# Optimization experiments

Measured on AMD Instinct MI355X. Metric: run time of the kernel, lower is better.

Reference implementation:

```python
import jax, jax.numpy as jnp
import numpy as np


def gcn_layer(h, src, dst, norm, W, b, num_nodes):
    # PyG GCNConv: linear transform, normalized scatter-add aggregation, then bias
    h = h @ W                                    # [N, out]
    msg = h[src] * norm[:, None]                 # [E+N, out] gathered messages
    out = jax.ops.segment_sum(msg, dst, num_segments=num_nodes)
    return out + b


def setup_inputs() -> dict:
    key = jax.random.key(0)
    ks = jax.random.split(key, 6)
    N, E, D, H, C = 100000, 1600000, 128, 64, 2
    x = jax.random.normal(ks[0], (N, D), dtype=jnp.float32)
    edge_index = jax.random.randint(ks[1], (2, E), 0, N, dtype=jnp.int64)
    def glorot(k, shape):
        lim = np.sqrt(6.0 / (shape[0] + shape[1]))
        return jax.random.uniform(k, shape, jnp.float32, -lim, lim)
    return {
        "x": x,
        "edge_index": edge_index,
        "W1": glorot(ks[2], (D, H)), "b1": jnp.zeros((H,), jnp.float32),
        "W2": glorot(ks[3], (H, H)), "b2": jnp.zeros((H,), jnp.float32),
        "W3": glorot(ks[4], (H, H)), "b3": jnp.zeros((H,), jnp.float32),
        "Wfc": glorot(ks[5], (H, C)), "bfc": jnp.zeros((C,), jnp.float32),
    }


def reference(x, edge_index, W1, b1, W2, b2, W3, b3, Wfc, bfc):
    N = x.shape[0]
    # add self loops (GCNConv default), symmetric deg^-1/2 normalization
    loops = jnp.arange(N, dtype=edge_index.dtype)
    src = jnp.concatenate([edge_index[0], loops])
    dst = jnp.concatenate([edge_index[1], loops])
    deg = jax.ops.segment_sum(jnp.ones_like(dst, dtype=x.dtype), dst, num_segments=N)
    dinv = jnp.where(deg > 0, jax.lax.rsqrt(deg), 0.0)
    norm = dinv[src] * dinv[dst]

    h = jax.nn.relu(gcn_layer(x, src, dst, norm, W1, b1, N))
    h = jax.nn.relu(gcn_layer(h, src, dst, norm, W2, b2, N))
    h = jax.nn.relu(gcn_layer(h, src, dst, norm, W3, b3, N))
    logits = h @ Wfc + bfc
    return jax.nn.log_softmax(logits, axis=1)
```

## Files before the change

### kernel.cpp

```cpp
#include <hip/hip_runtime.h>
#include <math.h>


static inline size_t alignup(size_t x){ return (x + 511) & ~size_t(511); }

typedef float v4f __attribute__((ext_vector_type(4)));
typedef unsigned short v4u16 __attribute__((ext_vector_type(4)));

__device__ __forceinline__ unsigned short f32_to_bf16(float f){
  union { float f; unsigned int u; } c; c.f = f;
  unsigned int u = c.u + 0x7FFFu + ((c.u >> 16) & 1u);
  return (unsigned short)(u >> 16);
}
__device__ __forceinline__ v4f bf16x4_to_f32(v4u16 a){
  union { unsigned int u; float f; } c0,c1,c2,c3;
  c0.u = (unsigned int)a.x << 16;
  c1.u = (unsigned int)a.y << 16;
  c2.u = (unsigned int)a.z << 16;
  c3.u = (unsigned int)a.w << 16;
  v4f r; r.x=c0.f; r.y=c1.f; r.z=c2.f; r.w=c3.f;
  return r;
}

#define NBUCK 1024
#define CHUNK 8192
#define CCAP  3584

__global__ void zero_kernel(int* __restrict__ p, int n){
  int i = blockIdx.x*256 + threadIdx.x;
  if(i<n) p[i] = 0;
}

__global__ __launch_bounds__(1024) void hist_kernel(const int* __restrict__ dst,
                                                    int* __restrict__ bcnt, int E){
  __shared__ int h[NBUCK];
  int t = threadIdx.x;
  h[t]=0;
  __syncthreads();
  int base = blockIdx.x*CHUNK;
  #pragma unroll
  for(int i=0;i<CHUNK;i+=1024){
    int e = base+i+t;
    if(e<E) atomicAdd(&h[dst[e]>>7], 1);
  }
  __syncthreads();
  if(h[t]) atomicAdd(&bcnt[t], h[t]);
}

__global__ void scan_buckets_kernel(const int* __restrict__ bcnt, int* __restrict__ bbase,
                                    int* __restrict__ bfill){
  __shared__ int sh[256];
  int t = threadIdx.x;
  int v0=bcnt[4*t], v1=bcnt[4*t+1], v2=bcnt[4*t+2], v3=bcnt[4*t+3];
  int ts = v0+v1+v2+v3;
  sh[t]=ts; __syncthreads();
  for(int off=1; off<256; off<<=1){
    int x=(t>=off)?sh[t-off]:0; __syncthreads();
    sh[t]+=x; __syncthreads();
  }
  int run = sh[t]-ts;
  int i0=4*t;
  bbase[i0+0]=run; bfill[i0+0]=run; run+=v0;
  bbase[i0+1]=run; bfill[i0+1]=run; run+=v1;
  bbase[i0+2]=run; bfill[i0+2]=run; run+=v2;
  bbase[i0+3]=run; bfill[i0+3]=run;
}

__global__ __launch_bounds__(1024) void scatter_kernel(const int* __restrict__ src,
                                                       const int* __restrict__ dst,
                                                       int* __restrict__ bfill,
                                                       int* __restrict__ pairs, int E){
  __shared__ int hist[NBUCK];
  __shared__ int delta[NBUCK];
  __shared__ int wsum[16];
  __shared__ int vals[CHUNK];
  __shared__ unsigned short bkt[CHUNK];
  int t = threadIdx.x;
  int lane = t & 63, wid = t >> 6;
  int cbase = blockIdx.x*CHUNK;
  hist[t]=0;
  __syncthreads();
  #pragma unroll
  for(int i=0;i<CHUNK;i+=1024){
    int e = cbase+i+t;
    if(e<E) atomicAdd(&hist[dst[e]>>7], 1);
  }
  __syncthreads();
  int v = hist[t];
  int x = v;
  #pragma unroll
  for(int off=1; off<64; off<<=1){
    int y = __shfl_up(x, off, 64);
    if(lane >= off) x += y;
  }
  if(lane==63) wsum[wid]=x;
  __syncthreads();
  if(wid==0){
    int s2 = (lane<16) ? wsum[lane] : 0;
    #pragma unroll
    for(int off=1; off<16; off<<=1){
      int y = __shfl_up(s2, off, 64);
      if(lane >= off) s2 += y;
    }
    if(lane<16) wsum[lane]=s2;
  }
  __syncthreads();
  int run = (x - v) + (wid ? wsum[wid-1] : 0);
  int g = v ? atomicAdd(&bfill[t], v) : 0;
  hist[t]=run; delta[t]=g-run;
  __syncthreads();
  #pragma unroll
  for(int i=0;i<CHUNK;i+=1024){
    int e = cbase+i+t;
    if(e<E){
      int d = dst[e];
      int b = d>>7;
      int slot = atomicAdd(&hist[b], 1);
      vals[slot] = ((d&127)<<17) | src[e];
      bkt[slot]  = (unsigned short)b;
    }
  }
  __syncthreads();
  int cnt = E - cbase; if(cnt > CHUNK) cnt = CHUNK;
  for(int i=t;i<cnt;i+=1024){
    int b = bkt[i];
    pairs[delta[b] + i] = vals[i];
  }
}

__global__ __launch_bounds__(256) void bucket_csr_kernel(const int* __restrict__ pairs,
                                                         const int* __restrict__ bbase,
                                                         int* __restrict__ row_ptr,
                                                         float* __restrict__ dinv,
                                                         int* __restrict__ col,
                                                         int N, int E){
  __shared__ int hist[128];
  __shared__ int pref[128];
  __shared__ int fill[128];
  __shared__ int srcs[CCAP];
  int b = blockIdx.x, t = threadIdx.x;
  int s = bbase[b], e = bbase[b+1];
  int cnt = e - s; if(cnt > CCAP) cnt = CCAP;
  if(t<128) hist[t]=0;
  __syncthreads();
  int v[CCAP/256];
  #pragma unroll
  for(int i=0;i<CCAP/256;i++){
    int idx = i*256 + t;
    if(idx<cnt){ v[i]=pairs[s+idx]; atomicAdd(&hist[v[i]>>17], 1); }
  }
  __syncthreads();
  if(t<128) pref[t]=hist[t];
  __syncthreads();
  for(int off=1; off<128; off<<=1){
    int x=0;
    if(t<128 && t>=off) x=pref[t-off];
    __syncthreads();
    if(t<128) pref[t]+=x;
    __syncthreads();
  }
  if(t<128){
    int ex = pref[t]-hist[t];
    fill[t]=ex;
    int node = b*128 + t;
    if(node<N){
      row_ptr[node] = s + ex;
      dinv[node] = rsqrtf((float)(hist[t]+1));
    }
  }
  if(b==0 && t==0) row_ptr[N]=E;
  __syncthreads();
  #pragma unroll
  for(int i=0;i<CCAP/256;i++){
    int idx = i*256 + t;
    if(idx<cnt){
      int ld = v[i]>>17;
      int pos = atomicAdd(&fill[ld], 1);
      srcs[pos] = v[i] & 0x1FFFF;
    }
  }
  __syncthreads();
  for(int i=t;i<cnt;i+=256) col[s+i]=srcs[i];
}

template<int K>
__global__ __launch_bounds__(256) void lin_kernel(const float* __restrict__ h,
                                                  const float* __restrict__ W,
                                                  const float* __restrict__ dinv,
                                                  unsigned short* __restrict__ g, int N){
  constexpr int TR = 32, RW = 8;
  __shared__ __align__(16) float hs[TR*K];
  __shared__ __align__(16) float ws[K*64];
  int t = threadIdx.x, wave = t>>6, lane = t&63;
  long rbase = (long)blockIdx.x*TR;
  const v4f* wsrc = (const v4f*)W;
  #pragma unroll
  for(int idx = t; idx < K*16; idx += 256)
    ((v4f*)ws)[idx] = wsrc[idx];
  const v4f* hsrc = (const v4f*)(h + rbase*K);
  if(rbase + TR <= N){
    #pragma unroll
    for(int idx = t; idx < TR*K/4; idx += 256)
      ((v4f*)hs)[idx] = hsrc[idx];
  } else {
    int lim = (int)((N - rbase)*K/4);
    for(int idx = t; idx < lim; idx += 256)
      ((v4f*)hs)[idx] = hsrc[idx];
  }
  __syncthreads();
  float acc[RW];
  #pragma unroll
  for(int r=0;r<RW;r++) acc[r]=0.f;
  const float* hw = hs + wave*RW*K;
  #pragma unroll 2
  for(int k=0;k<K;k+=4){
    float w0 = ws[(k+0)*64+lane];
    float w1 = ws[(k+1)*64+lane];
    float w2 = ws[(k+2)*64+lane];
    float w3 = ws[(k+3)*64+lane];
    #pragma unroll
    for(int r=0;r<RW;r++){
      v4f hv = *(const v4f*)&hw[r*K+k];
      acc[r] = fmaf(hv.w, w3, fmaf(hv.z, w2, fmaf(hv.y, w1, fmaf(hv.x, w0, acc[r]))));
    }
  }
  long row0 = rbase + wave*RW;
  #pragma unroll
  for(int r=0;r<RW;r++){
    if(row0 + r < N)
      g[(row0+r)*64 + lane] = f32_to_bf16(dinv[row0+r]*acc[r]);
  }
}

__device__ __forceinline__ v4f gather_row4(const unsigned short* __restrict__ g,
                                           const int* __restrict__ col,
                                           int n, int s, int e, int l){
  v4f acc = bf16x4_to_f32(*(const v4u16*)&g[(size_t)n*64 + l*4]);
  for(int i = s; i < e; i += 16){
    int rem = e - i;
    int myc = (l < rem) ? col[i + l] : n;
    #pragma unroll
    for(int j0 = 0; j0 < 16; j0 += 4){
      int c0 = __shfl(myc, j0+0, 16);
      int c1 = __shfl(myc, j0+1, 16);
      int c2 = __shfl(myc, j0+2, 16);
      int c3 = __shfl(myc, j0+3, 16);
      v4f x0 = bf16x4_to_f32(*(const v4u16*)&g[(size_t)c0*64 + l*4]);
      v4f x1 = bf16x4_to_f32(*(const v4u16*)&g[(size_t)c1*64 + l*4]);
      v4f x2 = bf16x4_to_f32(*(const v4u16*)&g[(size_t)c2*64 + l*4]);
      v4f x3 = bf16x4_to_f32(*(const v4u16*)&g[(size_t)c3*64 + l*4]);
      float m0 = (j0+0 < rem) ? 1.f : 0.f;
      float m1 = (j0+1 < rem) ? 1.f : 0.f;
      float m2 = (j0+2 < rem) ? 1.f : 0.f;
      float m3 = (j0+3 < rem) ? 1.f : 0.f;
      acc.x = fmaf(m0,x0.x, fmaf(m1,x1.x, fmaf(m2,x2.x, fmaf(m3,x3.x, acc.x))));
      acc.y = fmaf(m0,x0.y, fmaf(m1,x1.y, fmaf(m2,x2.y, fmaf(m3,x3.y, acc.y))));
      acc.z = fmaf(m0,x0.z, fmaf(m1,x1.z, fmaf(m2,x2.z, fmaf(m3,x3.z, acc.z))));
      acc.w = fmaf(m0,x0.w, fmaf(m1,x1.w, fmaf(m2,x2.w, fmaf(m3,x3.w, acc.w))));
      if(j0+4 >= rem) break;
    }
  }
  return acc;
}

__global__ __launch_bounds__(256) void agg_lin_kernel(const unsigned short* __restrict__ g,
                                                      const int* __restrict__ row_ptr,
                                                      const int* __restrict__ col,
                                                      const float* __restrict__ dinv,
                                                      const float* __restrict__ bias,
                                                      const float* __restrict__ W,
                                                      unsigned short* __restrict__ g2,
                                                      int N){
  __shared__ __align__(16) float hsh[16*64];
  __shared__ __align__(16) float ws[64*64];
  int t = threadIdx.x, wave = t>>6, lane = t&63;
  int l = lane & 15, q = lane >> 4;
  #pragma unroll
  for(int idx = t; idx < 1024; idx += 256)
    ((v4f*)ws)[idx] = ((const v4f*)W)[idx];
  int n = blockIdx.x*16 + wave*4 + q;
  bool valid = n < N;
  int nn = valid ? n : (N-1);
  int s = row_ptr[nn], e = row_ptr[nn+1];
  v4f acc = gather_row4(g, col, nn, s, e, l);
  float dv = dinv[nn];
  v4f bs = *(const v4f*)&bias[l*4];
  v4f hv;
  hv.x = fmaxf(fmaf(dv, acc.x, bs.x), 0.f);
  hv.y = fmaxf(fmaf(dv, acc.y, bs.y), 0.f);
  hv.z = fmaxf(fmaf(dv, acc.z, bs.z), 0.f);
  hv.w = fmaxf(fmaf(dv, acc.w, bs.w), 0.f);
  *(v4f*)&hsh[(wave*4+q)*64 + l*4] = hv;
  __syncthreads();
  const float* hrow = &hsh[wave*4*64];
  float o0=0.f, o1=0.f, o2=0.f, o3=0.f;
  #pragma unroll 4
  for(int k=0;k<64;k++){
    float w = ws[k*64 + lane];
    o0 = fmaf(hrow[k],       w, o0);
    o1 = fmaf(hrow[64+k],    w, o1);
    o2 = fmaf(hrow[128+k],   w, o2);
    o3 = fmaf(hrow[192+k],   w, o3);
  }
  int base = blockIdx.x*16 + wave*4;
  if(base+0 < N) g2[(size_t)(base+0)*64 + lane] = f32_to_bf16(dinv[base+0]*o0);
  if(base+1 < N) g2[(size_t)(base+1)*64 + lane] = f32_to_bf16(dinv[base+1]*o1);
  if(base+2 < N) g2[(size_t)(base+2)*64 + lane] = f32_to_bf16(dinv[base+2]*o2);
  if(base+3 < N) g2[(size_t)(base+3)*64 + lane] = f32_to_bf16(dinv[base+3]*o3);
}

__global__ __launch_bounds__(256) void agg_final_kernel(const unsigned short* __restrict__ g,
                                                        const int* __restrict__ row_ptr,
                                                        const int* __restrict__ col,
                                                        const float* __restrict__ dinv,
                                                        const float* __restrict__ bias,
                                                        const float* __restrict__ Wfc,
                                                        const float* __restrict__ bfc,
                                                        float* __restrict__ out, int N){
  int t = threadIdx.x, wave = t>>6, lane = t&63;
  int l = lane & 15, q = lane >> 4;
  int n = blockIdx.x*16 + wave*4 + q;
  bool valid = n < N;
  if(!valid) n = N-1;
  int s = row_ptr[n], e = row_ptr[n+1];
  v4f acc = gather_row4(g, col, n, s, e, l);
  float dv = dinv[n];
  v4f bs = *(const v4f*)&bias[l*4];
  v4f hv;
  hv.x = fmaxf(fmaf(dv, acc.x, bs.x), 0.f);
  hv.y = fmaxf(fmaf(dv, acc.y, bs.y), 0.f);
  hv.z = fmaxf(fmaf(dv, acc.z, bs.z), 0.f);
  hv.w = fmaxf(fmaf(dv, acc.w, bs.w), 0.f);
  v4f wa = *(const v4f*)&Wfc[l*8];
  v4f wb = *(const v4f*)&Wfc[l*8+4];
  float p0 = hv.x*wa.x + hv.y*wa.z + hv.z*wb.x + hv.w*wb.z;
  float p1 = hv.x*wa.y + hv.y*wa.w + hv.z*wb.y + hv.w*wb.w;
  for(int off=8; off; off>>=1){
    p0 += __shfl_down(p0, off, 16);
    p1 += __shfl_down(p1, off, 16);
  }
  if(valid && l==0){
    float l0 = p0 + bfc[0], l1 = p1 + bfc[1];
    float m  = fmaxf(l0, l1);
    float lse = m + logf(expf(l0-m) + expf(l1-m));
    out[(size_t)n*2+0] = l0 - lse;
    out[(size_t)n*2+1] = l1 - lse;
  }
}

extern "C" void kernel_launch(void* const* d_in, const int* in_sizes, int n_in,
                              void* d_out, int out_size, void* d_ws, size_t ws_size,
                              hipStream_t stream) {
  (void)n_in; (void)out_size; (void)ws_size;
  const float* x   = (const float*)d_in[0];
  const int*   ei  = (const int*)  d_in[1];
  const float* W1  = (const float*)d_in[2];
  const float* b1  = (const float*)d_in[3];
  const float* W2  = (const float*)d_in[4];
  const float* b2  = (const float*)d_in[5];
  const float* W3  = (const float*)d_in[6];
  const float* b3  = (const float*)d_in[7];
  const float* Wfc = (const float*)d_in[8];
  const float* bfc = (const float*)d_in[9];
  float* out = (float*)d_out;

  const int N = in_sizes[0] / 128;
  const int E = in_sizes[1] / 2;
  const int* src = ei;
  const int* dst = ei + E;
  const int NB = (N + 127) / 128;

  char* w = (char*)d_ws;
  int*   bcnt    = (int*)  w; w += alignup((size_t)NBUCK*4);
  int*   bbase   = (int*)  w; w += alignup((size_t)(NBUCK+1)*4);
  int*   bfill   = (int*)  w; w += alignup((size_t)NBUCK*4);
  int*   pairs   = (int*)  w; w += alignup((size_t)E*4);
  int*   row_ptr = (int*)  w; w += alignup((size_t)(N+1)*4);
  float* dinv    = (float*)w; w += alignup((size_t)N*4);
  int*   col     = (int*)  w; w += alignup((size_t)E*4);
  unsigned short* gA = (unsigned short*)w; w += alignup((size_t)N*64*2);
  unsigned short* gB = (unsigned short*)w; w += alignup((size_t)N*64*2);

  const int nblkE   = (E + CHUNK - 1) / CHUNK;
  const int nblkLin = (N + 31) / 32;
  const int nblkAgg = (N + 15) / 16;

  zero_kernel<<<(NBUCK+255)/256, 256, 0, stream>>>(bcnt, NBUCK);
  hist_kernel<<<nblkE, 1024, 0, stream>>>(dst, bcnt, E);
  scan_buckets_kernel<<<1, 256, 0, stream>>>(bcnt, bbase, bfill);
  scatter_kernel<<<nblkE, 1024, 0, stream>>>(src, dst, bfill, pairs, E);
  bucket_csr_kernel<<<NB, 256, 0, stream>>>(pairs, bbase, row_ptr, dinv, col, N, E);

  lin_kernel<128><<<nblkLin, 256, 0, stream>>>(x, W1, dinv, gA, N);
  agg_lin_kernel<<<nblkAgg, 256, 0, stream>>>(gA, row_ptr, col, dinv, b1, W2, gB, N);
  agg_lin_kernel<<<nblkAgg, 256, 0, stream>>>(gB, row_ptr, col, dinv, b2, W3, gA, N);
  agg_final_kernel<<<nblkAgg, 256, 0, stream>>>(gA, row_ptr, col, dinv, b3,
                                                Wfc, bfc, out, N);
}
```

Before: 291.4 us.

## Use bf16 MFMA for first-layer linear and zero-row padding in gather

Replaces the scalar FP32 first-layer matmul (x @ W1) with a bf16 MFMA 16x16x32 kernel. W1 is pre-packed into per-lane fragments by a small new kernel, and x is converted to bf16 on the fly. The gather loop drops its per-edge mask FMAs: out-of-range neighbour slots now point at an extra zeroed padding row N in each feature buffer, so they can be added unconditionally. This adds three tiny launches and lowers the first-layer input precision to bf16.

```diff
diff --git a/kernel.cpp b/kernel.cpp
--- a/kernel.cpp
+++ b/kernel.cpp
@@ -6,6 +6,8 @@
 
 typedef float v4f __attribute__((ext_vector_type(4)));
 typedef unsigned short v4u16 __attribute__((ext_vector_type(4)));
+typedef __attribute__((ext_vector_type(8))) short short8;
+typedef __attribute__((ext_vector_type(4))) float f32x4;
 
 __device__ __forceinline__ unsigned short f32_to_bf16(float f){
   union { float f; unsigned int u; } c; c.f = f;
@@ -29,6 +31,21 @@
 __global__ void zero_kernel(int* __restrict__ p, int n){
   int i = blockIdx.x*256 + threadIdx.x;
   if(i<n) p[i] = 0;
+}
+
+__global__ void wfrag_kernel(const float* __restrict__ W,
+                             unsigned short* __restrict__ wf, int ksteps){
+  int t = threadIdx.x + blockIdx.x*256;
+  int total = ksteps*4*64;
+  if(t >= total) return;
+  int l  = t & 63;
+  int nb = (t>>6) & 3;
+  int ks = t>>8;
+  int k0 = ks*32 + 8*(l>>4);
+  int n  = nb*16 + (l&15);
+  unsigned short* o = wf + (size_t)t*8;
+  #pragma unroll
+  for(int i=0;i<8;i++) o[i] = f32_to_bf16(W[(size_t)(k0+i)*64 + n]);
 }
 
 __global__ __launch_bounds__(1024) void hist_kernel(const int* __restrict__ dst,
@@ -183,62 +200,59 @@
   for(int i=t;i<cnt;i+=256) col[s+i]=srcs[i];
 }
 
-template<int K>
-__global__ __launch_bounds__(256) void lin_kernel(const float* __restrict__ h,
-                                                  const float* __restrict__ W,
-                                                  const float* __restrict__ dinv,
-                                                  unsigned short* __restrict__ g, int N){
-  constexpr int TR = 32, RW = 8;
-  __shared__ __align__(16) float hs[TR*K];
-  __shared__ __align__(16) float ws[K*64];
+__global__ __launch_bounds__(256) void lin_mfma_kernel(const float* __restrict__ x,
+                                                       const unsigned short* __restrict__ wf,
+                                                       const float* __restrict__ dinv,
+                                                       unsigned short* __restrict__ g,
+                                                       int N){
+  __shared__ __align__(16) unsigned short wl[4*4*64*8];
   int t = threadIdx.x, wave = t>>6, lane = t&63;
-  long rbase = (long)blockIdx.x*TR;
-  const v4f* wsrc = (const v4f*)W;
-  #pragma unroll
-  for(int idx = t; idx < K*16; idx += 256)
-    ((v4f*)ws)[idx] = wsrc[idx];
-  const v4f* hsrc = (const v4f*)(h + rbase*K);
-  if(rbase + TR <= N){
-    #pragma unroll
-    for(int idx = t; idx < TR*K/4; idx += 256)
-      ((v4f*)hs)[idx] = hsrc[idx];
-  } else {
-    int lim = (int)((N - rbase)*K/4);
-    for(int idx = t; idx < lim; idx += 256)
-      ((v4f*)hs)[idx] = hsrc[idx];
-  }
-  __syncthreads();
-  float acc[RW];
-  #pragma unroll
-  for(int r=0;r<RW;r++) acc[r]=0.f;
-  const float* hw = hs + wave*RW*K;
-  #pragma unroll 2
-  for(int k=0;k<K;k+=4){
-    float w0 = ws[(k+0)*64+lane];
-    float w1 = ws[(k+1)*64+lane];
-    float w2 = ws[(k+2)*64+lane];
-    float w3 = ws[(k+3)*64+lane];
-    #pragma unroll
-    for(int r=0;r<RW;r++){
-      v4f hv = *(const v4f*)&hw[r*K+k];
-      acc[r] = fmaf(hv.w, w3, fmaf(hv.z, w2, fmaf(hv.y, w1, fmaf(hv.x, w0, acc[r]))));
-    }
-  }
-  long row0 = rbase + wave*RW;
-  #pragma unroll
-  for(int r=0;r<RW;r++){
-    if(row0 + r < N)
-      g[(row0+r)*64 + lane] = f32_to_bf16(dinv[row0+r]*acc[r]);
+  #pragma unroll
+  for(int idx=t; idx<1024; idx+=256)
+    ((v4f*)wl)[idx] = ((const v4f*)wf)[idx];
+  __syncthreads();
+  int row = blockIdx.x*64 + wave*16 + (lane&15);
+  int arow = row < N ? row : N-1;
+  const float* xr = x + (size_t)arow*128 + 8*(lane>>4);
+  f32x4 acc0={0.f,0.f,0.f,0.f}, acc1=acc0, acc2=acc0, acc3=acc0;
+  #pragma unroll
+  for(int ks=0; ks<4; ks++){
+    v4f a0 = *(const v4f*)(xr + ks*32);
+    v4f a1 = *(const v4f*)(xr + ks*32 + 4);
+    short8 af;
+    af[0]=(short)f32_to_bf16(a0.x); af[1]=(short)f32_to_bf16(a0.y);
+    af[2]=(short)f32_to_bf16(a0.z); af[3]=(short)f32_to_bf16(a0.w);
+    af[4]=(short)f32_to_bf16(a1.x); af[5]=(short)f32_to_bf16(a1.y);
+    af[6]=(short)f32_to_bf16(a1.z); af[7]=(short)f32_to_bf16(a1.w);
+    const short8* wb = ((const short8*)wl) + ks*256 + lane;
+    acc0 = __builtin_amdgcn_mfma_f32_16x16x32_bf16(af, wb[0],   acc0, 0, 0, 0);
+    acc1 = __builtin_amdgcn_mfma_f32_16x16x32_bf16(af, wb[64],  acc1, 0, 0, 0);
+    acc2 = __builtin_amdgcn_mfma_f32_16x16x32_bf16(af, wb[128], acc2, 0, 0, 0);
+    acc3 = __builtin_amdgcn_mfma_f32_16x16x32_bf16(af, wb[192], acc3, 0, 0, 0);
+  }
+  int rbase = blockIdx.x*64 + wave*16 + (lane>>4)*4;
+  int c = lane & 15;
+  #pragma unroll
+  for(int j=0;j<4;j++){
+    int r = rbase + j;
+    if(r < N){
+      float dv = dinv[r];
+      unsigned short* go = g + (size_t)r*64 + c;
+      go[0]  = f32_to_bf16(dv*acc0[j]);
+      go[16] = f32_to_bf16(dv*acc1[j]);
+      go[32] = f32_to_bf16(dv*acc2[j]);
+      go[48] = f32_to_bf16(dv*acc3[j]);
+    }
   }
 }
 
 __device__ __forceinline__ v4f gather_row4(const unsigned short* __restrict__ g,
                                            const int* __restrict__ col,
-                                           int n, int s, int e, int l){
+                                           int n, int s, int e, int l, int ZR){
   v4f acc = bf16x4_to_f32(*(const v4u16*)&g[(size_t)n*64 + l*4]);
   for(int i = s; i < e; i += 16){
     int rem = e - i;
-    int myc = (l < rem) ? col[i + l] : n;
+    int myc = (l < rem) ? col[i + l] : ZR;
     #pragma unroll
     for(int j0 = 0; j0 < 16; j0 += 4){
       int c0 = __shfl(myc, j0+0, 16);
@@ -249,14 +263,10 @@
       v4f x1 = bf16x4_to_f32(*(const v4u16*)&g[(size_t)c1*64 + l*4]);
       v4f x2 = bf16x4_to_f32(*(const v4u16*)&g[(size_t)c2*64 + l*4]);
       v4f x3 = bf16x4_to_f32(*(const v4u16*)&g[(size_t)c3*64 + l*4]);
-      float m0 = (j0+0 < rem) ? 1.f : 0.f;
-      float m1 = (j0+1 < rem) ? 1.f : 0.f;
-      float m2 = (j0+2 < rem) ? 1.f : 0.f;
-      float m3 = (j0+3 < rem) ? 1.f : 0.f;
-      acc.x = fmaf(m0,x0.x, fmaf(m1,x1.x, fmaf(m2,x2.x, fmaf(m3,x3.x, acc.x))));
-      acc.y = fmaf(m0,x0.y, fmaf(m1,x1.y, fmaf(m2,x2.y, fmaf(m3,x3.y, acc.y))));
-      acc.z = fmaf(m0,x0.z, fmaf(m1,x1.z, fmaf(m2,x2.z, fmaf(m3,x3.z, acc.z))));
-      acc.w = fmaf(m0,x0.w, fmaf(m1,x1.w, fmaf(m2,x2.w, fmaf(m3,x3.w, acc.w))));
+      acc.x += (x0.x + x1.x) + (x2.x + x3.x);
+      acc.y += (x0.y + x1.y) + (x2.y + x3.y);
+      acc.z += (x0.z + x1.z) + (x2.z + x3.z);
+      acc.w += (x0.w + x1.w) + (x2.w + x3.w);
       if(j0+4 >= rem) break;
     }
   }
@@ -282,7 +292,7 @@
   bool valid = n < N;
   int nn = valid ? n : (N-1);
   int s = row_ptr[nn], e = row_ptr[nn+1];
-  v4f acc = gather_row4(g, col, nn, s, e, l);
+  v4f acc = gather_row4(g, col, nn, s, e, l, N);
   float dv = dinv[nn];
   v4f bs = *(const v4f*)&bias[l*4];
   v4f hv;
@@ -323,7 +333,7 @@
   bool valid = n < N;
   if(!valid) n = N-1;
   int s = row_ptr[n], e = row_ptr[n+1];
-  v4f acc = gather_row4(g, col, n, s, e, l);
+  v4f acc = gather_row4(g, col, n, s, e, l, N);
   float dv = dinv[n];
   v4f bs = *(const v4f*)&bias[l*4];
   v4f hv;
@@ -378,20 +388,25 @@
   int*   row_ptr = (int*)  w; w += alignup((size_t)(N+1)*4);
   float* dinv    = (float*)w; w += alignup((size_t)N*4);
   int*   col     = (int*)  w; w += alignup((size_t)E*4);
-  unsigned short* gA = (unsigned short*)w; w += alignup((size_t)N*64*2);
-  unsigned short* gB = (unsigned short*)w; w += alignup((size_t)N*64*2);
+  unsigned short* gA = (unsigned short*)w; w += alignup((size_t)(N+1)*64*2);
+  unsigned short* gB = (unsigned short*)w; w += alignup((size_t)(N+1)*64*2);
+  unsigned short* wf1 = (unsigned short*)w; w += alignup((size_t)4*4*64*8*2);
 
   const int nblkE   = (E + CHUNK - 1) / CHUNK;
-  const int nblkLin = (N + 31) / 32;
+  const int nblkLin = (N + 63) / 64;
   const int nblkAgg = (N + 15) / 16;
 
   zero_kernel<<<(NBUCK+255)/256, 256, 0, stream>>>(bcnt, NBUCK);
+  zero_kernel<<<1, 256, 0, stream>>>((int*)(gA + (size_t)N*64), 32);
+  zero_kernel<<<1, 256, 0, stream>>>((int*)(gB + (size_t)N*64), 32);
+  wfrag_kernel<<<4, 256, 0, stream>>>(W1, wf1, 4);
+
   hist_kernel<<<nblkE, 1024, 0, stream>>>(dst, bcnt, E);
   scan_buckets_kernel<<<1, 256, 0, stream>>>(bcnt, bbase, bfill);
   scatter_kernel<<<nblkE, 1024, 0, stream>>>(src, dst, bfill, pairs, E);
   bucket_csr_kernel<<<NB, 256, 0, stream>>>(pairs, bbase, row_ptr, dinv, col, N, E);
 
-  lin_kernel<128><<<nblkLin, 256, 0, stream>>>(x, W1, dinv, gA, N);
+  lin_mfma_kernel<<<nblkLin, 256, 0, stream>>>(x, wf1, dinv, gA, N);
   agg_lin_kernel<<<nblkAgg, 256, 0, stream>>>(gA, row_ptr, col, dinv, b1, W2, gB, N);
   agg_lin_kernel<<<nblkAgg, 256, 0, stream>>>(gB, row_ptr, col, dinv, b2, W3, gA, N);
   agg_final_kernel<<<nblkAgg, 256, 0, stream>>>(gA, row_ptr, col, dinv, b3,
```

Measured after the change: 263.6 us. -9.5%, faster.
